# Kernel tuning notes

Hardware: AMD Instinct MI355X
Metric: run time of the kernel (lower is better)

## Reference

```python
import jax, jax.numpy as jnp
import numpy as np

EPSILON = 1e-8
B, T, H = 4, 4096, 2048          # batch, seq, hidden_dim
D, NH, K = 256, 4, 32            # belief_dim, num_heads, top_k
NB, NG = 65536, 16               # n_beliefs, n_goals
NEG_INF = -1e30


def setup_inputs() -> dict:
    key = jax.random.key(0)
    ks = jax.random.split(key, 8)
    hidden = jax.random.normal(ks[0], (B, T, H), dtype=jnp.float32)
    beliefs = jax.random.normal(ks[1], (NB, D), dtype=jnp.float32)
    active_mask = jax.random.bernoulli(ks[2], 0.5, (NB,))
    goal_embeddings = jax.random.normal(ks[3], (NG, D), dtype=jnp.float32)
    goal_priorities = jax.random.uniform(ks[4], (NG,), dtype=jnp.float32)
    # torch nn.Linear weights are [out_features, in_features]
    Wq = jax.random.normal(ks[5], (NH * D, H), dtype=jnp.float32) / np.float32(np.sqrt(H))
    Wo = jax.random.normal(ks[6], (H, NH * D), dtype=jnp.float32) / np.float32(np.sqrt(NH * D))
    log_temperature = jax.random.normal(ks[7], (NH,), dtype=jnp.float32) * 0.1
    return {"hidden": hidden, "beliefs": beliefs, "active_mask": active_mask,
            "goal_embeddings": goal_embeddings, "goal_priorities": goal_priorities,
            "Wq": Wq, "Wo": Wo, "log_temperature": log_temperature}


def reference(hidden, beliefs, active_mask, goal_embeddings, goal_priorities, Wq, Wo, log_temperature):
    # --- rough-score top-k pre-filter over active beliefs (N_active > top_k path) ---
    mean_query = hidden.mean(axis=(0, 1))                      # [H]
    rough_query = (Wq @ mean_query).reshape(NH, D).mean(axis=0)  # [D]
    radii = jnp.maximum(jnp.linalg.norm(beliefs, axis=-1), EPSILON)  # [NB]
    angles = beliefs / radii[:, None]                          # [NB, D]
    rough_scores = angles @ rough_query                        # [NB]
    # mask-gather: inactive beliefs get -inf so topk selects only active ones
    rough_scores = jnp.where(active_mask, rough_scores, NEG_INF)
    _, topk_idx = jax.lax.top_k(rough_scores, K)               # [K]
    active_beliefs = beliefs[topk_idx]                         # [K, D]

    # --- angle-normalized keys, raw values ---
    a_radii = jnp.maximum(jnp.linalg.norm(active_beliefs, axis=-1), EPSILON)
    keys = active_beliefs / a_radii[:, None]                   # [K, D]
    values = active_beliefs                                    # [K, D]

    # --- per-head queries and temperature ---
    queries = (hidden @ Wq.T).reshape(B, T, NH, D)             # [B,T,h,D]
    temperature = jnp.maximum(jnp.exp(log_temperature), 0.1)   # [h]
    scores = jnp.einsum('bthd,nd->bthn', queries, keys) / np.float32(np.sqrt(D))
    scores = scores * temperature[None, None, :, None]         # [B,T,h,K]

    # --- goal-similarity bias ---
    g_radii = jnp.maximum(jnp.linalg.norm(goal_embeddings, axis=-1), EPSILON)
    goal_angles = goal_embeddings / g_radii[:, None]           # [NG, D]
    sim = (keys @ goal_angles.T) * goal_priorities[None, :]    # [K, NG]
    goal_bias = sim.max(axis=-1)                               # [K], same for all heads
    scores = scores + goal_bias[None, None, None, :]

    attn = jax.nn.softmax(scores, axis=-1)                     # [B,T,h,K]
    retrieved = jnp.einsum('bthn,nd->bthd', attn, values).reshape(B, T, NH * D)
    return retrieved @ Wo.T                                    # [B,T,H]
```

## Files before the change

### kernel.cpp

```cpp
#include <hip/hip_runtime.h>

typedef unsigned int u32;
typedef unsigned short u16;
typedef unsigned long long u64;

typedef __bf16 bf16x8 __attribute__((ext_vector_type(8)));
typedef float f32x4 __attribute__((ext_vector_type(4)));

#define DEV __device__ __forceinline__

DEV u16 f2bf(float f) {
  u32 u = __float_as_uint(f);
  u += 0x7fffu + ((u >> 16) & 1u);
  return (u16)(u >> 16);
}

DEV void gld_lds16(const void* g, void* l) {
  __builtin_amdgcn_global_load_lds((const __attribute__((address_space(1))) u32*)g,
                                   (__attribute__((address_space(3))) u32*)l, 16, 0, 0);
}

DEV u64 packkey(float f, u32 idx) {
  u32 u = __float_as_uint(f);
  u = (u & 0x80000000u) ? ~u : (u | 0x80000000u);
  return ((u64)u << 32) | (u32)(~idx);
}

__global__ __launch_bounds__(64) void k_detect(const u32* m, int* flag) {
  u64 b = __ballot(m[threadIdx.x] > 1u);
  if (threadIdx.x == 0) *flag = (b == 0ull) ? 1 : 0;
}

__global__ __launch_bounds__(256) void k_conv_mean(const float4* __restrict__ hidden4,
                                                   ushort4* __restrict__ hb4,
                                                   float4* __restrict__ partial4) {
  const int c4 = blockIdx.x * 256 + threadIdx.x;
  const int r0 = blockIdx.y * 256;
  float4 s = {0.f, 0.f, 0.f, 0.f};
  for (int r = 0; r < 256; r++) {
    float4 v = hidden4[(size_t)(r0 + r) * 512 + c4];
    ushort4 o; o.x = f2bf(v.x); o.y = f2bf(v.y); o.z = f2bf(v.z); o.w = f2bf(v.w);
    hb4[(size_t)(r0 + r) * 512 + c4] = o;
    s.x += v.x; s.y += v.y; s.z += v.z; s.w += v.w;
  }
  partial4[blockIdx.y * 512 + c4] = s;
}

__global__ __launch_bounds__(256) void k_mean(const float* __restrict__ partial,
                                              float* __restrict__ mean) {
  const int col = blockIdx.x * 256 + threadIdx.x;
  float s = 0.f;
  for (int c = 0; c < 64; c++) s += partial[c * 2048 + col];
  mean[col] = s * (1.0f / 16384.0f);
}

__global__ __launch_bounds__(256) void k_rq(const float* __restrict__ Wq,
                                            const float* __restrict__ mean,
                                            float* __restrict__ rq) {
  const int w = threadIdx.x >> 6, l = threadIdx.x & 63;
  const int row = blockIdx.x * 4 + w;
  float s = 0.f;
#pragma unroll
  for (int j = 0; j < 32; j++)
    s = fmaf(Wq[(size_t)row * 2048 + j * 64 + l], mean[j * 64 + l], s);
  for (int mk = 1; mk < 64; mk <<= 1) s += __shfl_xor(s, mk);
  if (l == 0) atomicAdd(&rq[row & 255], 0.25f * s);
}

__global__ __launch_bounds__(256) void k_rough(const float* __restrict__ beliefs,
                                               const void* __restrict__ amask,
                                               const int* __restrict__ flag,
                                               const float* __restrict__ rq,
                                               u64* __restrict__ keys) {
  const int t = threadIdx.x, w = t >> 6, l = t & 63;
  const int n = blockIdx.x * 4 + w;
  float4 b = *(const float4*)(beliefs + (size_t)n * 256 + l * 4);
  float4 qv = *(const float4*)(rq + l * 4);
  float dot = b.x * qv.x + b.y * qv.y + b.z * qv.z + b.w * qv.w;
  float ss = b.x * b.x + b.y * b.y + b.z * b.z + b.w * b.w;
  for (int mk = 1; mk < 64; mk <<= 1) { dot += __shfl_xor(dot, mk); ss += __shfl_xor(ss, mk); }
  if (l == 0) {
    bool act = (*flag) ? (((const int*)amask)[n] != 0)
                       : (((const unsigned char*)amask)[n] != 0);
    float score = act ? dot / fmaxf(sqrtf(ss), 1e-8f) : -1e30f;
    keys[n] = packkey(score, (u32)n);
  }
}

__global__ __launch_bounds__(256) void k_topk(const u64* __restrict__ in, int cnt,
                                              u64* __restrict__ outk, int* __restrict__ outi) {
  __shared__ u64 buf[2048];
  __shared__ u64 wmaxS[4];
  const int t = threadIdx.x;
  const int slots = cnt >> 8;
  const u64* src = in + (size_t)blockIdx.x * cnt;
  for (int i = 0; i < slots; i++) buf[t + i * 256] = src[t + i * 256];
  __syncthreads();
  const int l = t & 63, w = t >> 6;
  for (int r = 0; r < 32; r++) {
    u64 m = 0;
    for (int i = 0; i < slots; i++) { u64 v = buf[t + i * 256]; m = v > m ? v : m; }
    for (int mk = 1; mk < 64; mk <<= 1) { u64 o = __shfl_xor(m, mk); m = o > m ? o : m; }
    if (l == 0) wmaxS[w] = m;
    __syncthreads();
    u64 a = wmaxS[0] > wmaxS[1] ? wmaxS[0] : wmaxS[1];
    u64 b = wmaxS[2] > wmaxS[3] ? wmaxS[2] : wmaxS[3];
    u64 win = a > b ? a : b;
    for (int i = 0; i < slots; i++) if (buf[t + i * 256] == win) buf[t + i * 256] = 0ull;
    if (t == 0) {
      if (outk) outk[blockIdx.x * 32 + r] = win;
      if (outi) outi[r] = (int)(~(u32)(win & 0xffffffffull));
    }
    __syncthreads();
  }
}

__global__ __launch_bounds__(256) void k_prep(const float* __restrict__ beliefs,
                                              const float* __restrict__ goals,
                                              const float* __restrict__ prio,
                                              const float* __restrict__ logt,
                                              const int* __restrict__ topk,
                                              float* __restrict__ keysf_g,
                                              float* __restrict__ valsf_g,
                                              float* __restrict__ biasO, float* __restrict__ tempO) {
  __shared__ float keysf[32 * 256];
  __shared__ float gradS[16];
  const int t = threadIdx.x, w = t >> 6, l = t & 63;
  for (int g = w * 4; g < w * 4 + 4; g++) {
    float4 v = *(const float4*)(goals + g * 256 + l * 4);
    float ss = v.x * v.x + v.y * v.y + v.z * v.z + v.w * v.w;
    for (int mk = 1; mk < 64; mk <<= 1) ss += __shfl_xor(ss, mk);
    if (l == 0) gradS[g] = fmaxf(sqrtf(ss), 1e-8f);
  }
  for (int kk = w * 8; kk < w * 8 + 8; kk++) {
    int idx = topk[kk];
    float4 v = *(const float4*)(beliefs + (size_t)idx * 256 + l * 4);
    float ss = v.x * v.x + v.y * v.y + v.z * v.z + v.w * v.w;
    for (int mk = 1; mk < 64; mk <<= 1) ss += __shfl_xor(ss, mk);
    float rr = 1.0f / fmaxf(sqrtf(ss), 1e-8f);
    float4 kv; kv.x = v.x * rr; kv.y = v.y * rr; kv.z = v.z * rr; kv.w = v.w * rr;
    *(float4*)&keysf[kk * 256 + l * 4] = kv;
    *(float4*)&keysf_g[kk * 256 + l * 4] = kv;
    *(float4*)&valsf_g[kk * 256 + l * 4] = v;
  }
  __syncthreads();
  for (int kk = w * 8; kk < w * 8 + 8; kk++) {
    float4 kv = *(const float4*)&keysf[kk * 256 + l * 4];
    float best = -1e30f;
    for (int g = 0; g < 16; g++) {
      float4 gv = *(const float4*)(goals + g * 256 + l * 4);
      float d = kv.x * gv.x + kv.y * gv.y + kv.z * gv.z + kv.w * gv.w;
      for (int mk = 1; mk < 64; mk <<= 1) d += __shfl_xor(d, mk);
      float sim = d / gradS[g] * prio[g];
      best = fmaxf(best, sim);
    }
    if (l == 0) biasO[kk] = best;
  }
  if (t < 4) tempO[t] = fmaxf(__expf(logt[t]), 0.1f);
}

__global__ __launch_bounds__(256) void k_build_kp(const float* __restrict__ Wq,
                                                  const float* __restrict__ keysf_g,
                                                  u16* __restrict__ Kp) {
  __shared__ float keysS[32 * 256];
  __shared__ float WqS[64 * 64];
  const int t = threadIdx.x;
  const int h = blockIdx.x;
  const int c0 = blockIdx.y * 64;
#pragma unroll
  for (int it = 0; it < 32; it++) keysS[t + it * 256] = keysf_g[t + it * 256];
  const int n0 = (t >> 5) * 4;
  const int c2 = (t & 31) * 2;
  float acc[4][2] = {};
  for (int dc = 0; dc < 4; dc++) {
    __syncthreads();
#pragma unroll
    for (int it = 0; it < 16; it++) {
      int i = t + it * 256;
      int r = i >> 6, c = i & 63;
      WqS[i] = Wq[(size_t)(h * 256 + dc * 64 + r) * 2048 + c0 + c];
    }
    __syncthreads();
    for (int d4 = 0; d4 < 16; d4++) {
      float4 kv[4];
#pragma unroll
      for (int i = 0; i < 4; i++)
        kv[i] = *(const float4*)&keysS[(n0 + i) * 256 + dc * 64 + d4 * 4];
#pragma unroll
      for (int dd = 0; dd < 4; dd++) {
        float2 w2 = *(const float2*)&WqS[(d4 * 4 + dd) * 64 + c2];
        float kvd[4] = {kv[0][dd], kv[1][dd], kv[2][dd], kv[3][dd]};
#pragma unroll
        for (int i = 0; i < 4; i++) {
          acc[i][0] = fmaf(kvd[i], w2.x, acc[i][0]);
          acc[i][1] = fmaf(kvd[i], w2.y, acc[i][1]);
        }
      }
    }
  }
#pragma unroll
  for (int i = 0; i < 4; i++) {
    u32 pk = (u32)f2bf(acc[i][0]) | ((u32)f2bf(acc[i][1]) << 16);
    *(u32*)&Kp[(size_t)(h * 32 + n0 + i) * 2048 + c0 + c2] = pk;
  }
}

__global__ __launch_bounds__(256) void k_build_vwo(const float* __restrict__ Wo,
                                                   const float* __restrict__ valsf_g,
                                                   u16* __restrict__ VWoT) {
  __shared__ float valsS[32 * 256];
  __shared__ float WoS[32 * 256];
  const int t = threadIdx.x;
  const int c0 = blockIdx.x * 32;
#pragma unroll
  for (int it = 0; it < 32; it++) valsS[t + it * 256] = valsf_g[t + it * 256];
  const int c = t >> 3;
  const int n0 = (t & 7) * 4;
  for (int h = 0; h < 4; h++) {
    __syncthreads();
#pragma unroll
    for (int it = 0; it < 32; it++) {
      int i = t + it * 256;
      int r = i >> 8, d = i & 255;
      WoS[i] = Wo[(size_t)(c0 + r) * 1024 + h * 256 + d];
    }
    __syncthreads();
    float acc[4] = {};
    for (int d4 = 0; d4 < 64; d4++) {
      float4 w4 = *(const float4*)&WoS[c * 256 + d4 * 4];
#pragma unroll
      for (int i = 0; i < 4; i++) {
        float4 kv = *(const float4*)&valsS[(n0 + i) * 256 + d4 * 4];
        acc[i] = fmaf(w4.x, kv.x, acc[i]);
        acc[i] = fmaf(w4.y, kv.y, acc[i]);
        acc[i] = fmaf(w4.z, kv.z, acc[i]);
        acc[i] = fmaf(w4.w, kv.w, acc[i]);
      }
    }
    ushort4 o; o.x = f2bf(acc[0]); o.y = f2bf(acc[1]); o.z = f2bf(acc[2]); o.w = f2bf(acc[3]);
    *(ushort4*)&VWoT[(size_t)(c0 + c) * 128 + h * 32 + n0] = o;
  }
}

__global__ __launch_bounds__(256) void k_gemm_nt(const u16* __restrict__ A,
                                                 const u16* __restrict__ B,
                                                 float* __restrict__ C,
                                                 int N, int lda, int ldb, int kcount, int M) {
  __shared__ __align__(16) u16 As[128 * 32];
  __shared__ __align__(16) u16 Bs[128 * 32];
  const int t = threadIdx.x;
  const int w = t >> 6, l = t & 63;
  const int m0 = blockIdx.y * 128, n0 = blockIdx.x * 128;
  const int p = blockIdx.z;
  const int wm = (w >> 1) * 64, wn = (w & 1) * 64;
  const int c = l & 15, q = l >> 4;
  f32x4 acc[4][4] = {};
  const int rsrc = w * 16 + (l >> 2);
  const int kc = (l & 3) * 8;
  const u16* Ab = A + (size_t)(m0 + rsrc) * lda + (size_t)p * kcount + kc;
  const u16* Bb = B + (size_t)(n0 + rsrc) * ldb + (size_t)p * kcount + kc;
  C += (size_t)p * M * N;
  u16* AsW = &As[w * 512];
  u16* BsW = &Bs[w * 512];
  for (int kt = 0; kt < kcount; kt += 32) {
    gld_lds16(Ab + kt, AsW);
    gld_lds16(Ab + (size_t)64 * lda + kt, AsW + 2048);
    gld_lds16(Bb + kt, BsW);
    gld_lds16(Bb + (size_t)64 * ldb + kt, BsW + 2048);
    __syncthreads();
    bf16x8 af[4], bfr[4];
#pragma unroll
    for (int i = 0; i < 4; i++)
      af[i] = __builtin_bit_cast(bf16x8, *(const uint4*)&As[(wm + i * 16 + c) * 32 + q * 8]);
#pragma unroll
    for (int i = 0; i < 4; i++)
      bfr[i] = __builtin_bit_cast(bf16x8, *(const uint4*)&Bs[(wn + i * 16 + c) * 32 + q * 8]);
#pragma unroll
    for (int mi = 0; mi < 4; mi++)
#pragma unroll
      for (int ni = 0; ni < 4; ni++)
        acc[mi][ni] = __builtin_amdgcn_mfma_f32_16x16x32_bf16(af[mi], bfr[ni], acc[mi][ni], 0, 0, 0);
    __syncthreads();
  }
#pragma unroll
  for (int mi = 0; mi < 4; mi++)
#pragma unroll
    for (int ni = 0; ni < 4; ni++)
#pragma unroll
      for (int r = 0; r < 4; r++) {
        int row = m0 + wm + mi * 16 + q * 4 + r;
        int col = n0 + wn + ni * 16 + c;
        C[(size_t)row * N + col] = acc[mi][ni][r];
      }
}

__global__ __launch_bounds__(256) void k_soft(const float* __restrict__ Sp,
                                              const float* __restrict__ bias,
                                              const float* __restrict__ temp,
                                              u16* __restrict__ P) {
  __shared__ float biasS[32];
  __shared__ float tS[4];
  const int t = threadIdx.x;
  if (t < 32) biasS[t] = bias[t];
  if (t < 4) tS[t] = temp[t];
  __syncthreads();
  const int w = t >> 6, l = t & 63;
  const int row = blockIdx.x * 4 + w;
  const size_t base = (size_t)row * 128;
  const size_t SPN = (size_t)16384 * 128;
  float s1 = Sp[base + l] + Sp[SPN + base + l] + Sp[2 * SPN + base + l] + Sp[3 * SPN + base + l];
  float s2 = Sp[base + 64 + l] + Sp[SPN + base + 64 + l] + Sp[2 * SPN + base + 64 + l] + Sp[3 * SPN + base + 64 + l];
  const int n = l & 31;
  float v1 = fmaf(s1, tS[l >> 5] * 0.0625f, biasS[n]);
  float v2 = fmaf(s2, tS[2 + (l >> 5)] * 0.0625f, biasS[n]);
  float m1 = v1, m2 = v2;
#pragma unroll
  for (int mk = 1; mk <= 16; mk <<= 1) { m1 = fmaxf(m1, __shfl_xor(m1, mk)); m2 = fmaxf(m2, __shfl_xor(m2, mk)); }
  float e1 = __expf(v1 - m1), e2 = __expf(v2 - m2);
  float q1 = e1, q2 = e2;
#pragma unroll
  for (int mk = 1; mk <= 16; mk <<= 1) { q1 += __shfl_xor(q1, mk); q2 += __shfl_xor(q2, mk); }
  P[base + l] = f2bf(e1 / q1);
  P[base + 64 + l] = f2bf(e2 / q2);
}

extern "C" void kernel_launch(void* const* d_in, const int* in_sizes, int n_in,
                              void* d_out, int out_size, void* d_ws, size_t ws_size,
                              hipStream_t stream) {
  const float* hidden = (const float*)d_in[0];
  const float* beliefs = (const float*)d_in[1];
  const void* amask = d_in[2];
  const float* goals = (const float*)d_in[3];
  const float* prio = (const float*)d_in[4];
  const float* Wq = (const float*)d_in[5];
  const float* Wo = (const float*)d_in[6];
  const float* logt = (const float*)d_in[7];
  float* out = (float*)d_out;

  char* ws = (char*)d_ws;
  size_t off = 0;
  auto alloc = [&](size_t bytes) { char* p = ws + off; off = (off + bytes + 255) & ~(size_t)255; return p; };
  u16* hb      = (u16*)alloc(67108864);
  float* Sp    = (float*)alloc(33554432);
  u16* P       = (u16*)alloc(4194304);
  u16* kp      = (u16*)alloc(524288);
  u16* vwot    = (u16*)alloc(524288);
  float* partial = (float*)alloc(524288);
  float* meanq = (float*)alloc(8192);
  float* rq    = (float*)alloc(1024);
  u64* keys    = (u64*)alloc(524288);
  u64* cands   = (u64*)alloc(16384);
  int* topkidx = (int*)alloc(128);
  float* keysf = (float*)alloc(32768);
  float* valsf = (float*)alloc(32768);
  float* biasv = (float*)alloc(128);
  float* tempv = (float*)alloc(16);
  int* flag    = (int*)alloc(16);

  hipMemsetAsync(rq, 0, 1024, stream);
  k_detect<<<1, 64, 0, stream>>>((const u32*)amask, flag);
  k_conv_mean<<<dim3(2, 64), 256, 0, stream>>>((const float4*)hidden, (ushort4*)hb, (float4*)partial);
  k_mean<<<8, 256, 0, stream>>>(partial, meanq);
  k_rq<<<256, 256, 0, stream>>>(Wq, meanq, rq);
  k_rough<<<16384, 256, 0, stream>>>(beliefs, amask, flag, rq, keys);
  k_topk<<<64, 256, 0, stream>>>(keys, 1024, cands, nullptr);
  k_topk<<<1, 256, 0, stream>>>(cands, 2048, nullptr, topkidx);
  k_prep<<<1, 256, 0, stream>>>(beliefs, goals, prio, logt, topkidx, keysf, valsf, biasv, tempv);
  k_build_kp<<<dim3(4, 32), 256, 0, stream>>>(Wq, keysf, kp);
  k_build_vwo<<<64, 256, 0, stream>>>(Wo, valsf, vwot);
  k_gemm_nt<<<dim3(1, 128, 4), 256, 0, stream>>>(hb, kp, Sp, 128, 2048, 2048, 512, 16384);
  k_soft<<<4096, 256, 0, stream>>>(Sp, biasv, tempv, P);
  k_gemm_nt<<<dim3(16, 128, 1), 256, 0, stream>>>(P, vwot, out, 2048, 128, 128, 128, 16384);
}
```

Measured before the change: 553.2 us.

## Widen conv/mean grid, fold mask detection into rough pass, store split-K partials as bf16

```diff
diff --git a/kernel.cpp b/kernel.cpp
--- a/kernel.cpp
+++ b/kernel.cpp
@@ -14,6 +14,7 @@
   u += 0x7fffu + ((u >> 16) & 1u);
   return (u16)(u >> 16);
 }
+DEV float bf2f(u16 u) { return __uint_as_float((u32)u << 16); }
 
 DEV void gld_lds16(const void* g, void* l) {
   __builtin_amdgcn_global_load_lds((const __attribute__((address_space(1))) u32*)g,
@@ -26,18 +27,13 @@
   return ((u64)u << 32) | (u32)(~idx);
 }
 
-__global__ __launch_bounds__(64) void k_detect(const u32* m, int* flag) {
-  u64 b = __ballot(m[threadIdx.x] > 1u);
-  if (threadIdx.x == 0) *flag = (b == 0ull) ? 1 : 0;
-}
-
 __global__ __launch_bounds__(256) void k_conv_mean(const float4* __restrict__ hidden4,
                                                    ushort4* __restrict__ hb4,
                                                    float4* __restrict__ partial4) {
   const int c4 = blockIdx.x * 256 + threadIdx.x;
-  const int r0 = blockIdx.y * 256;
+  const int r0 = blockIdx.y * 64;
   float4 s = {0.f, 0.f, 0.f, 0.f};
-  for (int r = 0; r < 256; r++) {
+  for (int r = 0; r < 64; r++) {
     float4 v = hidden4[(size_t)(r0 + r) * 512 + c4];
     ushort4 o; o.x = f2bf(v.x); o.y = f2bf(v.y); o.z = f2bf(v.z); o.w = f2bf(v.w);
     hb4[(size_t)(r0 + r) * 512 + c4] = o;
@@ -48,10 +44,19 @@
 
 __global__ __launch_bounds__(256) void k_mean(const float* __restrict__ partial,
                                               float* __restrict__ mean) {
-  const int col = blockIdx.x * 256 + threadIdx.x;
-  float s = 0.f;
-  for (int c = 0; c < 64; c++) s += partial[c * 2048 + col];
-  mean[col] = s * (1.0f / 16384.0f);
+  __shared__ float red[256];
+  const int t = threadIdx.x;
+  const int c = t & 15, s = t >> 4;
+  const int col = blockIdx.x * 16 + c;
+  float acc = 0.f;
+  for (int ch = s; ch < 256; ch += 16) acc += partial[ch * 2048 + col];
+  red[t] = acc;
+  __syncthreads();
+  for (int st = 8; st > 0; st >>= 1) {
+    if (s < st) red[t] += red[t + st * 16];
+    __syncthreads();
+  }
+  if (s == 0) mean[col] = red[c] * (1.0f / 16384.0f);
 }
 
 __global__ __launch_bounds__(256) void k_rq(const float* __restrict__ Wq,
@@ -69,19 +74,20 @@
 
 __global__ __launch_bounds__(256) void k_rough(const float* __restrict__ beliefs,
                                                const void* __restrict__ amask,
-                                               const int* __restrict__ flag,
                                                const float* __restrict__ rq,
                                                u64* __restrict__ keys) {
   const int t = threadIdx.x, w = t >> 6, l = t & 63;
   const int n = blockIdx.x * 4 + w;
+  u32 mv = ((const u32*)amask)[l];
+  bool isInt = (__ballot(mv > 1u) == 0ull);
   float4 b = *(const float4*)(beliefs + (size_t)n * 256 + l * 4);
   float4 qv = *(const float4*)(rq + l * 4);
   float dot = b.x * qv.x + b.y * qv.y + b.z * qv.z + b.w * qv.w;
   float ss = b.x * b.x + b.y * b.y + b.z * b.z + b.w * b.w;
   for (int mk = 1; mk < 64; mk <<= 1) { dot += __shfl_xor(dot, mk); ss += __shfl_xor(ss, mk); }
   if (l == 0) {
-    bool act = (*flag) ? (((const int*)amask)[n] != 0)
-                       : (((const unsigned char*)amask)[n] != 0);
+    bool act = isInt ? (((const int*)amask)[n] != 0)
+                     : (((const unsigned char*)amask)[n] != 0);
     float score = act ? dot / fmaxf(sqrtf(ss), 1e-8f) : -1e30f;
     keys[n] = packkey(score, (u32)n);
   }
@@ -242,9 +248,10 @@
   }
 }
 
+template <typename OutT>
 __global__ __launch_bounds__(256) void k_gemm_nt(const u16* __restrict__ A,
                                                  const u16* __restrict__ B,
-                                                 float* __restrict__ C,
+                                                 OutT* __restrict__ C,
                                                  int N, int lda, int ldb, int kcount, int M) {
   __shared__ __align__(16) u16 As[128 * 32];
   __shared__ __align__(16) u16 Bs[128 * 32];
@@ -290,11 +297,13 @@
       for (int r = 0; r < 4; r++) {
         int row = m0 + wm + mi * 16 + q * 4 + r;
         int col = n0 + wn + ni * 16 + c;
-        C[(size_t)row * N + col] = acc[mi][ni][r];
+        float v = acc[mi][ni][r];
+        if constexpr (sizeof(OutT) == 2) C[(size_t)row * N + col] = (OutT)f2bf(v);
+        else                             C[(size_t)row * N + col] = v;
       }
 }
 
-__global__ __launch_bounds__(256) void k_soft(const float* __restrict__ Sp,
+__global__ __launch_bounds__(256) void k_soft(const u16* __restrict__ Sp,
                                               const float* __restrict__ bias,
                                               const float* __restrict__ temp,
                                               u16* __restrict__ P) {
@@ -308,8 +317,10 @@
   const int row = blockIdx.x * 4 + w;
   const size_t base = (size_t)row * 128;
   const size_t SPN = (size_t)16384 * 128;
-  float s1 = Sp[base + l] + Sp[SPN + base + l] + Sp[2 * SPN + base + l] + Sp[3 * SPN + base + l];
-  float s2 = Sp[base + 64 + l] + Sp[SPN + base + 64 + l] + Sp[2 * SPN + base + 64 + l] + Sp[3 * SPN + base + 64 + l];
+  float s1 = bf2f(Sp[base + l]) + bf2f(Sp[SPN + base + l])
+           + bf2f(Sp[2 * SPN + base + l]) + bf2f(Sp[3 * SPN + base + l]);
+  float s2 = bf2f(Sp[base + 64 + l]) + bf2f(Sp[SPN + base + 64 + l])
+           + bf2f(Sp[2 * SPN + base + 64 + l]) + bf2f(Sp[3 * SPN + base + 64 + l]);
   const int n = l & 31;
   float v1 = fmaf(s1, tS[l >> 5] * 0.0625f, biasS[n]);
   float v2 = fmaf(s2, tS[2 + (l >> 5)] * 0.0625f, biasS[n]);
@@ -341,11 +352,11 @@
   size_t off = 0;
   auto alloc = [&](size_t bytes) { char* p = ws + off; off = (off + bytes + 255) & ~(size_t)255; return p; };
   u16* hb      = (u16*)alloc(67108864);
-  float* Sp    = (float*)alloc(33554432);
+  u16* Sp      = (u16*)alloc(16777216);
   u16* P       = (u16*)alloc(4194304);
   u16* kp      = (u16*)alloc(524288);
   u16* vwot    = (u16*)alloc(524288);
-  float* partial = (float*)alloc(524288);
+  float* partial = (float*)alloc(2097152);
   float* meanq = (float*)alloc(8192);
   float* rq    = (float*)alloc(1024);
   u64* keys    = (u64*)alloc(524288);
@@ -355,20 +366,18 @@
   float* valsf = (float*)alloc(32768);
   float* biasv = (float*)alloc(128);
   float* tempv = (float*)alloc(16);
-  int* flag    = (int*)alloc(16);
 
   hipMemsetAsync(rq, 0, 1024, stream);
-  k_detect<<<1, 64, 0, stream>>>((const u32*)amask, flag);
-  k_conv_mean<<<dim3(2, 64), 256, 0, stream>>>((const float4*)hidden, (ushort4*)hb, (float4*)partial);
-  k_mean<<<8, 256, 0, stream>>>(partial, meanq);
+  k_conv_mean<<<dim3(2, 256), 256, 0, stream>>>((const float4*)hidden, (ushort4*)hb, (float4*)partial);
+  k_mean<<<128, 256, 0, stream>>>(partial, meanq);
   k_rq<<<256, 256, 0, stream>>>(Wq, meanq, rq);
-  k_rough<<<16384, 256, 0, stream>>>(beliefs, amask, flag, rq, keys);
+  k_rough<<<16384, 256, 0, stream>>>(beliefs, amask, rq, keys);
   k_topk<<<64, 256, 0, stream>>>(keys, 1024, cands, nullptr);
   k_topk<<<1, 256, 0, stream>>>(cands, 2048, nullptr, topkidx);
   k_prep<<<1, 256, 0, stream>>>(beliefs, goals, prio, logt, topkidx, keysf, valsf, biasv, tempv);
   k_build_kp<<<dim3(4, 32), 256, 0, stream>>>(Wq, keysf, kp);
   k_build_vwo<<<64, 256, 0, stream>>>(Wo, valsf, vwot);
-  k_gemm_nt<<<dim3(1, 128, 4), 256, 0, stream>>>(hb, kp, Sp, 128, 2048, 2048, 512, 16384);
+  k_gemm_nt<u16><<<dim3(1, 128, 4), 256, 0, stream>>>(hb, kp, Sp, 128, 2048, 2048, 512, 16384);
   k_soft<<<4096, 256, 0, stream>>>(Sp, biasv, tempv, P);
-  k_gemm_nt<<<dim3(16, 128, 1), 256, 0, stream>>>(P, vwot, out, 2048, 128, 128, 128, 16384);
-}
+  k_gemm_nt<float><<<dim3(16, 128, 1), 256, 0, stream>>>(P, vwot, out, 2048, 128, 128, 128, 16384);
+}
```

Measured after the change: 538.2 us. 1.03x faster.
